# Optimization experiments

Measured on AMD Instinct MI355X. Metric: run time of the kernel, lower is better.

Reference implementation:

```python
import jax, jax.numpy as jnp
import numpy as np

B, T, C = 4, 2048, 1024
H = 16
D = C // H  # 64


def setup_inputs() -> dict:
    key = jax.random.key(0)
    ks = jax.random.split(key, 3)
    scale = 1.0 / np.sqrt(C)
    return {
        "x": jax.random.normal(ks[0], (B, T, C), dtype=jnp.float32),
        "W_attn": jax.random.normal(ks[1], (C, 3 * C), dtype=jnp.float32) * scale,
        "b_attn": jnp.zeros((3 * C,), dtype=jnp.float32),
        "W_proj": jax.random.normal(ks[2], (C, C), dtype=jnp.float32) * scale,
        "b_proj": jnp.zeros((C,), dtype=jnp.float32),
    }


def reference(x, W_attn, b_attn, W_proj, b_proj):
    b, t, c = x.shape
    qkv = x @ W_attn + b_attn                      # [B,T,3C]
    q, k, v = jnp.split(qkv, 3, axis=-1)           # each [B,T,C]
    to_heads = lambda z: z.reshape(b, t, H, D).transpose(0, 2, 1, 3)  # [B,H,T,D]
    q, k, v = to_heads(q), to_heads(k), to_heads(v)
    scores = jnp.einsum("bhtd,bhsd->bhts", q, k) / jnp.sqrt(jnp.float32(D))
    causal = jnp.tril(jnp.ones((t, t), dtype=bool))  # [T,T]
    scores = jnp.where(causal[None, None], scores, jnp.finfo(scores.dtype).min)
    attn = jax.nn.softmax(scores, axis=-1)           # [B,H,T,T]
    out = jnp.einsum("bhts,bhsd->bhtd", attn, v)     # [B,H,T,D]
    out = out.transpose(0, 2, 1, 3).reshape(b, t, c)
    return out @ W_proj + b_proj
```

## Files before the change

### kernel.cpp

```cpp
#include <hip/hip_runtime.h>
#include <hip/hip_bf16.h>

typedef __bf16 bf16_t;
typedef __attribute__((ext_vector_type(8))) __bf16 bf16x8;
typedef __attribute__((ext_vector_type(4))) float f32x4;
typedef __attribute__((ext_vector_type(4))) unsigned short u16x4;

#define B_DIM 4
#define T_DIM 2048
#define C_DIM 1024
#define H_DIM 16
#define D_DIM 64
#define M_TOK (B_DIM * T_DIM)
#define N_QKV (3 * C_DIM)
#define NT    (T_DIM / 64)
#define KSTR  72
#define CSC   0.18033688011112042f

__global__ void cvt_f32_to_bf16(const float* __restrict__ in, bf16_t* __restrict__ out, int n4) {
  int i = blockIdx.x * blockDim.x + threadIdx.x;
  if (i >= n4) return;
  float4 v = ((const float4*)in)[i];
  struct alignas(8) bv4 { bf16_t x, y, z, w; };
  bv4 o;
  o.x = (bf16_t)v.x; o.y = (bf16_t)v.y; o.z = (bf16_t)v.z; o.w = (bf16_t)v.w;
  ((bv4*)out)[i] = o;
}

__global__ void transpose_f32_to_bf16(const float* __restrict__ in, bf16_t* __restrict__ out,
                                      int K, int N) {
  __shared__ float tile[32][33];
  int bx = blockIdx.x * 32;
  int by = blockIdx.y * 32;
  int tx = threadIdx.x, ty = threadIdx.y;
#pragma unroll
  for (int i = 0; i < 32; i += 8)
    tile[ty + i][tx] = in[(size_t)(by + ty + i) * N + bx + tx];
  __syncthreads();
#pragma unroll
  for (int i = 0; i < 32; i += 8)
    out[(size_t)(bx + ty + i) * K + by + tx] = (bf16_t)tile[tx][ty + i];
}

#define BM 128
#define BN 128
#define BK 32
#define BKP 40

__global__ __launch_bounds__(256)
void gemm_bt_bias(const bf16_t* __restrict__ A, const bf16_t* __restrict__ Bt,
                  const float* __restrict__ bias, bf16_t* __restrict__ Cb,
                  float* __restrict__ Cf, int M, int N, int K) {
  __shared__ alignas(16) bf16_t As[BM * BKP];
  __shared__ alignas(16) bf16_t Bs[BN * BKP];
  const int tid = threadIdx.x;
  const int lane = tid & 63;
  const int wave = tid >> 6;
  const int wr = (wave >> 1) * 64, wc = (wave & 1) * 64;
  const int quad = lane >> 4, l16 = lane & 15;
  const int row0 = blockIdx.x * BM, col0 = blockIdx.y * BN;

  f32x4 acc[4][4];
#pragma unroll
  for (int i = 0; i < 4; ++i)
#pragma unroll
    for (int j = 0; j < 4; ++j)
      acc[i][j] = (f32x4){0.f, 0.f, 0.f, 0.f};

  for (int k0 = 0; k0 < K; k0 += BK) {
    __syncthreads();
#pragma unroll
    for (int c = tid; c < (BM * BK) / 8; c += 256) {
      int r = c >> 2, ck = (c & 3) * 8;
      *(bf16x8*)&As[r * BKP + ck] = *(const bf16x8*)&A[(size_t)(row0 + r) * K + k0 + ck];
      *(bf16x8*)&Bs[r * BKP + ck] = *(const bf16x8*)&Bt[(size_t)(col0 + r) * K + k0 + ck];
    }
    __syncthreads();
    bf16x8 af[4], bfr[4];
#pragma unroll
    for (int i = 0; i < 4; ++i)
      af[i] = *(const bf16x8*)&As[(wr + i * 16 + l16) * BKP + quad * 8];
#pragma unroll
    for (int j = 0; j < 4; ++j)
      bfr[j] = *(const bf16x8*)&Bs[(wc + j * 16 + l16) * BKP + quad * 8];
#pragma unroll
    for (int i = 0; i < 4; ++i)
#pragma unroll
      for (int j = 0; j < 4; ++j)
        acc[i][j] = __builtin_amdgcn_mfma_f32_16x16x32_bf16(af[i], bfr[j], acc[i][j], 0, 0, 0);
  }

#pragma unroll
  for (int i = 0; i < 4; ++i)
#pragma unroll
    for (int j = 0; j < 4; ++j) {
      int col = col0 + wc + j * 16 + l16;
      float bv = bias[col];
#pragma unroll
      for (int r = 0; r < 4; ++r) {
        int row = row0 + wr + i * 16 + quad * 4 + r;
        float v = acc[i][j][r] + bv;
        if (Cb) Cb[(size_t)row * N + col] = (bf16_t)v;
        else    Cf[(size_t)row * N + col] = v;
      }
    }
}

__device__ __forceinline__ void softmax_step(f32x4 sv[4], float& m_st, float& l_st,
                                             f32x4 o_acc[4], bool diag, bf16_t* PsW,
                                             int l16, int quad, int wave) {
  if (diag) {
    const int qr = wave * 16 + l16;
#pragma unroll
    for (int ct = 0; ct < 4; ++ct)
#pragma unroll
      for (int r = 0; r < 4; ++r)
        if (ct * 16 + quad * 4 + r > qr) sv[ct][r] = -INFINITY;
  }
  float rmax = sv[0][0];
#pragma unroll
  for (int ct = 0; ct < 4; ++ct)
#pragma unroll
    for (int r = 0; r < 4; ++r) rmax = fmaxf(rmax, sv[ct][r]);
  rmax = fmaxf(rmax, __shfl_xor(rmax, 16));
  rmax = fmaxf(rmax, __shfl_xor(rmax, 32));
  float m_new = fmaxf(m_st, rmax);
  float alpha = __builtin_amdgcn_exp2f((m_st - m_new) * CSC);
  float mc = m_new * CSC;
  float rsum = 0.f;
#pragma unroll
  for (int ct = 0; ct < 4; ++ct) {
    u16x4 pk;
#pragma unroll
    for (int r = 0; r < 4; ++r) {
      float p = __builtin_amdgcn_exp2f(__builtin_fmaf(sv[ct][r], CSC, -mc));
      rsum += p;
      pk[r] = __builtin_bit_cast(unsigned short, (bf16_t)p);
    }
    *(u16x4*)&PsW[l16 * KSTR + ct * 16 + quad * 4] = pk;
  }
  rsum += __shfl_xor(rsum, 16);
  rsum += __shfl_xor(rsum, 32);
  l_st = l_st * alpha + rsum;
  m_st = m_new;
#pragma unroll
  for (int dt = 0; dt < 4; ++dt)
#pragma unroll
    for (int r = 0; r < 4; ++r) o_acc[dt][r] *= alpha;
}

__global__ __launch_bounds__(256, 4)
void attn_fwd(const bf16_t* __restrict__ qkv, bf16_t* __restrict__ out) {
  __shared__ alignas(16) bf16_t Ks[64 * KSTR];
  __shared__ alignas(16) bf16_t Vt[64 * KSTR];
  __shared__ alignas(16) bf16_t Ps[4 * 2 * 16 * KSTR];

  const int tid = threadIdx.x;
  const int lane = tid & 63;
  const int wave = tid >> 6;
  const int quad = lane >> 4, l16 = lane & 15;
  const int qlo = blockIdx.x;
  const int qhi = NT - 1 - qlo;
  const int h = blockIdx.y, b = blockIdx.z;
  const size_t tokBase = (size_t)b * T_DIM;

  const bf16_t* qpl = qkv + (tokBase + qlo * 64 + wave * 16 + l16) * N_QKV + h * D_DIM;
  const bf16_t* qph = qkv + (tokBase + qhi * 64 + wave * 16 + l16) * N_QKV + h * D_DIM;
  bf16x8 ql0 = *(const bf16x8*)(qpl + quad * 8);
  bf16x8 ql1 = *(const bf16x8*)(qpl + 32 + quad * 8);
  bf16x8 qh0 = *(const bf16x8*)(qph + quad * 8);
  bf16x8 qh1 = *(const bf16x8*)(qph + 32 + quad * 8);

  f32x4 ol[4], oh[4];
#pragma unroll
  for (int dt = 0; dt < 4; ++dt) {
    ol[dt] = (f32x4){0.f, 0.f, 0.f, 0.f};
    oh[dt] = (f32x4){0.f, 0.f, 0.f, 0.f};
  }
  float ml = -INFINITY, ll = 0.f, mh = -INFINITY, lh = 0.f;

  const int tx = tid & 15, ty = tid >> 4;
  bf16_t* PsL = &Ps[(wave * 2 + 0) * 16 * KSTR];
  bf16_t* PsH = &Ps[(wave * 2 + 1) * 16 * KSTR];
  const f32x4 zero4 = (f32x4){0.f, 0.f, 0.f, 0.f};

  for (int t = 0; t <= qhi; ++t) {
    const bool lo = (t <= qlo);
    __syncthreads();
    {
      const bf16_t* kb = qkv + (tokBase + t * 64 + ty * 4) * N_QKV + h * D_DIM + C_DIM + tx * 4;
      u16x4 kv[4], vv[4];
#pragma unroll
      for (int r = 0; r < 4; ++r) kv[r] = *(const u16x4*)(kb + (size_t)r * N_QKV);
#pragma unroll
      for (int r = 0; r < 4; ++r) vv[r] = *(const u16x4*)(kb + (size_t)r * N_QKV + C_DIM);
#pragma unroll
      for (int r = 0; r < 4; ++r)
        *(u16x4*)&Ks[(ty * 4 + r) * KSTR + tx * 4] = kv[r];
#pragma unroll
      for (int i = 0; i < 4; ++i) {
        u16x4 p = (u16x4){vv[0][i], vv[1][i], vv[2][i], vv[3][i]};
        *(u16x4*)&Vt[(tx * 4 + i) * KSTR + ty * 4] = p;
      }
    }
    __syncthreads();

    f32x4 svl[4], svh[4];
#pragma unroll
    for (int ct = 0; ct < 4; ++ct) {
      bf16x8 kf0 = *(const bf16x8*)&Ks[(ct * 16 + l16) * KSTR + quad * 8];
      bf16x8 kf1 = *(const bf16x8*)&Ks[(ct * 16 + l16) * KSTR + 32 + quad * 8];
      if (lo) {
        svl[ct] = __builtin_amdgcn_mfma_f32_16x16x32_bf16(kf0, ql0, zero4, 0, 0, 0);
        svl[ct] = __builtin_amdgcn_mfma_f32_16x16x32_bf16(kf1, ql1, svl[ct], 0, 0, 0);
      }
      svh[ct] = __builtin_amdgcn_mfma_f32_16x16x32_bf16(kf0, qh0, zero4, 0, 0, 0);
      svh[ct] = __builtin_amdgcn_mfma_f32_16x16x32_bf16(kf1, qh1, svh[ct], 0, 0, 0);
    }

    if (lo) softmax_step(svl, ml, ll, ol, t == qlo, PsL, l16, quad, wave);
    softmax_step(svh, mh, lh, oh, t == qhi, PsH, l16, quad, wave);

    bf16x8 pl0, pl1, ph0, ph1;
    if (lo) {
      pl0 = *(const bf16x8*)&PsL[l16 * KSTR + quad * 8];
      pl1 = *(const bf16x8*)&PsL[l16 * KSTR + 32 + quad * 8];
    }
    ph0 = *(const bf16x8*)&PsH[l16 * KSTR + quad * 8];
    ph1 = *(const bf16x8*)&PsH[l16 * KSTR + 32 + quad * 8];
#pragma unroll
    for (int dt = 0; dt < 4; ++dt) {
      bf16x8 vf0 = *(const bf16x8*)&Vt[(dt * 16 + l16) * KSTR + quad * 8];
      bf16x8 vf1 = *(const bf16x8*)&Vt[(dt * 16 + l16) * KSTR + 32 + quad * 8];
      if (lo) {
        ol[dt] = __builtin_amdgcn_mfma_f32_16x16x32_bf16(vf0, pl0, ol[dt], 0, 0, 0);
        ol[dt] = __builtin_amdgcn_mfma_f32_16x16x32_bf16(vf1, pl1, ol[dt], 0, 0, 0);
      }
      oh[dt] = __builtin_amdgcn_mfma_f32_16x16x32_bf16(vf0, ph0, oh[dt], 0, 0, 0);
      oh[dt] = __builtin_amdgcn_mfma_f32_16x16x32_bf16(vf1, ph1, oh[dt], 0, 0, 0);
    }
  }

  struct alignas(8) bh4 { bf16_t a, b, c, d; };
  {
    float rl = 1.0f / ll;
    bf16_t* op = out + (tokBase + qlo * 64 + wave * 16 + l16) * C_DIM + h * D_DIM;
#pragma unroll
    for (int dt = 0; dt < 4; ++dt) {
      bh4 v = {(bf16_t)(ol[dt][0] * rl), (bf16_t)(ol[dt][1] * rl),
               (bf16_t)(ol[dt][2] * rl), (bf16_t)(ol[dt][3] * rl)};
      *(bh4*)(op + dt * 16 + quad * 4) = v;
    }
  }
  {
    float rl = 1.0f / lh;
    bf16_t* op = out + (tokBase + qhi * 64 + wave * 16 + l16) * C_DIM + h * D_DIM;
#pragma unroll
    for (int dt = 0; dt < 4; ++dt) {
      bh4 v = {(bf16_t)(oh[dt][0] * rl), (bf16_t)(oh[dt][1] * rl),
               (bf16_t)(oh[dt][2] * rl), (bf16_t)(oh[dt][3] * rl)};
      *(bh4*)(op + dt * 16 + quad * 4) = v;
    }
  }
}

extern "C" void kernel_launch(void* const* d_in, const int* in_sizes, int n_in,
                              void* d_out, int out_size, void* d_ws, size_t ws_size,
                              hipStream_t stream) {
  const float* x      = (const float*)d_in[0];
  const float* W_attn = (const float*)d_in[1];
  const float* b_attn = (const float*)d_in[2];
  const float* W_proj = (const float*)d_in[3];
  const float* b_proj = (const float*)d_in[4];
  float* out = (float*)d_out;

  char* ws = (char*)d_ws;
  bf16_t* xb   = (bf16_t*)ws;  ws += (size_t)M_TOK * C_DIM * 2;
  bf16_t* Wat  = (bf16_t*)ws;  ws += (size_t)N_QKV * C_DIM * 2;
  bf16_t* Wpt  = (bf16_t*)ws;  ws += (size_t)C_DIM * C_DIM * 2;
  bf16_t* qkv  = (bf16_t*)ws;  ws += (size_t)M_TOK * N_QKV * 2;
  bf16_t* attn = (bf16_t*)ws;  ws += (size_t)M_TOK * C_DIM * 2;

  {
    int n4 = (M_TOK * C_DIM) / 4;
    cvt_f32_to_bf16<<<n4 / 256, 256, 0, stream>>>(x, xb, n4);
  }
  transpose_f32_to_bf16<<<dim3(N_QKV / 32, C_DIM / 32), dim3(32, 8), 0, stream>>>(W_attn, Wat, C_DIM, N_QKV);
  transpose_f32_to_bf16<<<dim3(C_DIM / 32, C_DIM / 32), dim3(32, 8), 0, stream>>>(W_proj, Wpt, C_DIM, C_DIM);

  gemm_bt_bias<<<dim3(M_TOK / BM, N_QKV / BN), 256, 0, stream>>>(
      xb, Wat, b_attn, qkv, nullptr, M_TOK, N_QKV, C_DIM);

  attn_fwd<<<dim3(NT / 2, H_DIM, B_DIM), 256, 0, stream>>>(qkv, attn);

  gemm_bt_bias<<<dim3(M_TOK / BM, C_DIM / BN), 256, 0, stream>>>(
      attn, Wpt, b_proj, nullptr, out, M_TOK, C_DIM, C_DIM);
}
```

Measured before the change: 304.0 us.

## Use direct global-to-LDS loads in GEMM and prefetch next K/V tile in attention

The GEMM tile loads now use global_load_lds to write bf16 data straight into unpadded shared memory, skipping the register round trip. The attention kernel register-prefetches the next K/V tile while the current one is computed, hiding global load latency. It also halves the P scratch buffer by reusing one per-wave region for both query tiles. The risks are LDS bank conflicts from dropping the GEMM padding, extra register pressure from the prefetch under the 4-blocks launch bound, and a possible race when the second softmax overwrites shared P before the first tile's fragments are read back.

```diff
diff --git a/kernel.cpp b/kernel.cpp
--- a/kernel.cpp
+++ b/kernel.cpp
@@ -17,6 +17,11 @@
 #define KSTR  72
 #define CSC   0.18033688011112042f
 
+__device__ __forceinline__ void gload_lds16(const bf16_t* g, bf16_t* l) {
+  __builtin_amdgcn_global_load_lds((const __attribute__((address_space(1))) void*)(g),
+                                   (__attribute__((address_space(3))) void*)(l), 16, 0, 0);
+}
+
 __global__ void cvt_f32_to_bf16(const float* __restrict__ in, bf16_t* __restrict__ out, int n4) {
   int i = blockIdx.x * blockDim.x + threadIdx.x;
   if (i >= n4) return;
@@ -45,14 +50,13 @@
 #define BM 128
 #define BN 128
 #define BK 32
-#define BKP 40
 
 __global__ __launch_bounds__(256)
 void gemm_bt_bias(const bf16_t* __restrict__ A, const bf16_t* __restrict__ Bt,
                   const float* __restrict__ bias, bf16_t* __restrict__ Cb,
                   float* __restrict__ Cf, int M, int N, int K) {
-  __shared__ alignas(16) bf16_t As[BM * BKP];
-  __shared__ alignas(16) bf16_t Bs[BN * BKP];
+  __shared__ alignas(16) bf16_t As[BM * BK];
+  __shared__ alignas(16) bf16_t Bs[BN * BK];
   const int tid = threadIdx.x;
   const int lane = tid & 63;
   const int wave = tid >> 6;
@@ -60,6 +64,13 @@
   const int quad = lane >> 4, l16 = lane & 15;
   const int row0 = blockIdx.x * BM, col0 = blockIdx.y * BN;
 
+  const int srow = wave * 32 + (lane >> 2);
+  const int scol = (lane & 3) * 8;
+  const bf16_t* Ag = A + (size_t)(row0 + srow) * K + scol;
+  const bf16_t* Bg = Bt + (size_t)(col0 + srow) * K + scol;
+  bf16_t* AsW = &As[(wave * 32) * BK];
+  bf16_t* BsW = &Bs[(wave * 32) * BK];
+
   f32x4 acc[4][4];
 #pragma unroll
   for (int i = 0; i < 4; ++i)
@@ -69,20 +80,18 @@
 
   for (int k0 = 0; k0 < K; k0 += BK) {
     __syncthreads();
-#pragma unroll
-    for (int c = tid; c < (BM * BK) / 8; c += 256) {
-      int r = c >> 2, ck = (c & 3) * 8;
-      *(bf16x8*)&As[r * BKP + ck] = *(const bf16x8*)&A[(size_t)(row0 + r) * K + k0 + ck];
-      *(bf16x8*)&Bs[r * BKP + ck] = *(const bf16x8*)&Bt[(size_t)(col0 + r) * K + k0 + ck];
-    }
+    gload_lds16(Ag + k0, AsW);
+    gload_lds16(Ag + k0 + (size_t)16 * K, AsW + 16 * BK);
+    gload_lds16(Bg + k0, BsW);
+    gload_lds16(Bg + k0 + (size_t)16 * K, BsW + 16 * BK);
     __syncthreads();
     bf16x8 af[4], bfr[4];
 #pragma unroll
     for (int i = 0; i < 4; ++i)
-      af[i] = *(const bf16x8*)&As[(wr + i * 16 + l16) * BKP + quad * 8];
+      af[i] = *(const bf16x8*)&As[(wr + i * 16 + l16) * BK + quad * 8];
 #pragma unroll
     for (int j = 0; j < 4; ++j)
-      bfr[j] = *(const bf16x8*)&Bs[(wc + j * 16 + l16) * BKP + quad * 8];
+      bfr[j] = *(const bf16x8*)&Bs[(wc + j * 16 + l16) * BK + quad * 8];
 #pragma unroll
     for (int i = 0; i < 4; ++i)
 #pragma unroll
@@ -153,7 +162,7 @@
 void attn_fwd(const bf16_t* __restrict__ qkv, bf16_t* __restrict__ out) {
   __shared__ alignas(16) bf16_t Ks[64 * KSTR];
   __shared__ alignas(16) bf16_t Vt[64 * KSTR];
-  __shared__ alignas(16) bf16_t Ps[4 * 2 * 16 * KSTR];
+  __shared__ alignas(16) bf16_t Ps[4 * 16 * KSTR];
 
   const int tid = threadIdx.x;
   const int lane = tid & 63;
@@ -180,30 +189,35 @@
   float ml = -INFINITY, ll = 0.f, mh = -INFINITY, lh = 0.f;
 
   const int tx = tid & 15, ty = tid >> 4;
-  bf16_t* PsL = &Ps[(wave * 2 + 0) * 16 * KSTR];
-  bf16_t* PsH = &Ps[(wave * 2 + 1) * 16 * KSTR];
+  bf16_t* PsW = &Ps[wave * 16 * KSTR];
   const f32x4 zero4 = (f32x4){0.f, 0.f, 0.f, 0.f};
+
+  u16x4 kreg[4], vreg[4];
+  const bf16_t* kb0 = qkv + (tokBase + ty * 4) * N_QKV + h * D_DIM + C_DIM + tx * 4;
+#pragma unroll
+  for (int r = 0; r < 4; ++r) kreg[r] = *(const u16x4*)(kb0 + (size_t)r * N_QKV);
+#pragma unroll
+  for (int r = 0; r < 4; ++r) vreg[r] = *(const u16x4*)(kb0 + (size_t)r * N_QKV + C_DIM);
 
   for (int t = 0; t <= qhi; ++t) {
     const bool lo = (t <= qlo);
     __syncthreads();
-    {
-      const bf16_t* kb = qkv + (tokBase + t * 64 + ty * 4) * N_QKV + h * D_DIM + C_DIM + tx * 4;
-      u16x4 kv[4], vv[4];
-#pragma unroll
-      for (int r = 0; r < 4; ++r) kv[r] = *(const u16x4*)(kb + (size_t)r * N_QKV);
-#pragma unroll
-      for (int r = 0; r < 4; ++r) vv[r] = *(const u16x4*)(kb + (size_t)r * N_QKV + C_DIM);
-#pragma unroll
-      for (int r = 0; r < 4; ++r)
-        *(u16x4*)&Ks[(ty * 4 + r) * KSTR + tx * 4] = kv[r];
-#pragma unroll
-      for (int i = 0; i < 4; ++i) {
-        u16x4 p = (u16x4){vv[0][i], vv[1][i], vv[2][i], vv[3][i]};
-        *(u16x4*)&Vt[(tx * 4 + i) * KSTR + ty * 4] = p;
-      }
+#pragma unroll
+    for (int r = 0; r < 4; ++r)
+      *(u16x4*)&Ks[(ty * 4 + r) * KSTR + tx * 4] = kreg[r];
+#pragma unroll
+    for (int i = 0; i < 4; ++i) {
+      u16x4 p = (u16x4){vreg[0][i], vreg[1][i], vreg[2][i], vreg[3][i]};
+      *(u16x4*)&Vt[(tx * 4 + i) * KSTR + ty * 4] = p;
     }
     __syncthreads();
+    if (t < qhi) {
+      const bf16_t* kb = qkv + (tokBase + (t + 1) * 64 + ty * 4) * N_QKV + h * D_DIM + C_DIM + tx * 4;
+#pragma unroll
+      for (int r = 0; r < 4; ++r) kreg[r] = *(const u16x4*)(kb + (size_t)r * N_QKV);
+#pragma unroll
+      for (int r = 0; r < 4; ++r) vreg[r] = *(const u16x4*)(kb + (size_t)r * N_QKV + C_DIM);
+    }
 
     f32x4 svl[4], svh[4];
 #pragma unroll
@@ -218,16 +232,16 @@
       svh[ct] = __builtin_amdgcn_mfma_f32_16x16x32_bf16(kf1, qh1, svh[ct], 0, 0, 0);
     }
 
-    if (lo) softmax_step(svl, ml, ll, ol, t == qlo, PsL, l16, quad, wave);
-    softmax_step(svh, mh, lh, oh, t == qhi, PsH, l16, quad, wave);
-
     bf16x8 pl0, pl1, ph0, ph1;
     if (lo) {
-      pl0 = *(const bf16x8*)&PsL[l16 * KSTR + quad * 8];
-      pl1 = *(const bf16x8*)&PsL[l16 * KSTR + 32 + quad * 8];
-    }
-    ph0 = *(const bf16x8*)&PsH[l16 * KSTR + quad * 8];
-    ph1 = *(const bf16x8*)&PsH[l16 * KSTR + 32 + quad * 8];
+      softmax_step(svl, ml, ll, ol, t == qlo, PsW, l16, quad, wave);
+      pl0 = *(const bf16x8*)&PsW[l16 * KSTR + quad * 8];
+      pl1 = *(const bf16x8*)&PsW[l16 * KSTR + 32 + quad * 8];
+    }
+    softmax_step(svh, mh, lh, oh, t == qhi, PsW, l16, quad, wave);
+    ph0 = *(const bf16x8*)&PsW[l16 * KSTR + quad * 8];
+    ph1 = *(const bf16x8*)&PsW[l16 * KSTR + 32 + quad * 8];
+
 #pragma unroll
     for (int dt = 0; dt < 4; ++dt) {
       bf16x8 vf0 = *(const bf16x8*)&Vt[(dt * 16 + l16) * KSTR + quad * 8];
```

After: 295.6 us. 1.03x faster.
